# Optimization experiments

Measured on AMD Instinct MI355X. Metric: run time of the kernel, lower is better.

The kernel has to match this reference:

```python
import jax, jax.numpy as jnp
import numpy as np

EPS = 1e-8
HIDDEN = 200


def _dsmall(n, d):
    # torch: d = d*(d>eps) + eps*(d<=eps); n/d
    return n / jnp.where(d > EPS, d, EPS)


def _mp_match(v1, v2, w):
    # v1: (B,S,H); v2: (B,S,H) or (B,H); w: (L,H) -> (B,S,L)
    wt = w.T[None, None]                      # (1,1,H,L)
    a = v1[..., None] * wt                    # (B,S,H,L)
    if v2.ndim == 2:
        v2 = jnp.broadcast_to(v2[:, None, :], v1.shape)
    b = v2[..., None] * wt                    # (B,S,H,L)
    dot = jnp.sum(a * b, axis=2)
    na = jnp.linalg.norm(a, axis=2)
    nb = jnp.linalg.norm(b, axis=2)
    return dot / jnp.maximum(na * nb, EPS)    # cosine_similarity over H


def _mp_pairwise(v1, v2, w):
    # v1: (B,S1,H); v2: (B,S2,H); w: (L,H) -> (B,S1,S2,L)
    a = v1[:, None] * w[None, :, None]        # (B,L,S1,H)
    b = v2[:, None] * w[None, :, None]        # (B,L,S2,H)
    na = jnp.linalg.norm(a, axis=3, keepdims=True)   # (B,L,S1,1)
    nb = jnp.linalg.norm(b, axis=3, keepdims=True)   # (B,L,S2,1)
    n = jnp.einsum('blph,blqh->blpq', a, b)
    d = na * jnp.swapaxes(nb, 2, 3)
    return jnp.transpose(_dsmall(n, d), (0, 2, 3, 1))


def _attention(v1, v2):
    # cosine-similarity matrix (B,S1,S2)
    n1 = jnp.linalg.norm(v1, axis=2, keepdims=True)           # (B,S1,1)
    n2 = jnp.linalg.norm(v2, axis=2, keepdims=True)           # (B,S2,1)
    a = jnp.einsum('bph,bqh->bpq', v1, v2)
    return _dsmall(a, n1 * jnp.swapaxes(n2, 1, 2))


def _matching(con_p, con_h, w1, w2, w3, w4, w5, w6, w7, w8):
    p_fw, p_bw = con_p[..., :HIDDEN], con_p[..., HIDDEN:]
    h_fw, h_bw = con_h[..., :HIDDEN], con_h[..., HIDDEN:]

    # 1) full matching
    mv_p_full_fw = _mp_match(p_fw, h_fw[:, -1, :], w1)
    mv_p_full_bw = _mp_match(p_bw, h_bw[:, 0, :], w2)
    mv_h_full_fw = _mp_match(h_fw, p_fw[:, -1, :], w1)
    mv_h_full_bw = _mp_match(h_bw, p_bw[:, 0, :], w2)

    # 2) maxpooling matching
    mv_max_fw = _mp_pairwise(p_fw, h_fw, w3)  # (B,S1,S2,L)
    mv_max_bw = _mp_pairwise(p_bw, h_bw, w4)
    mv_p_max_fw = jnp.max(mv_max_fw, axis=2)
    mv_p_max_bw = jnp.max(mv_max_bw, axis=2)
    mv_h_max_fw = jnp.max(mv_max_fw, axis=1)
    mv_h_max_bw = jnp.max(mv_max_bw, axis=1)

    # 3) attentive matching (mean)
    att_fw = _attention(p_fw, h_fw)           # (B,S1,S2)
    att_bw = _attention(p_bw, h_bw)

    # sum of att_h over dim 2 is a matmul (same math, no (B,S1,S2,H) tensor)
    att_h_sum_fw = jnp.einsum('bpq,bqh->bph', att_fw, h_fw)
    att_h_sum_bw = jnp.einsum('bpq,bqh->bph', att_bw, h_bw)
    att_p_sum_fw = jnp.einsum('bpq,bph->bqh', att_fw, p_fw)
    att_p_sum_bw = jnp.einsum('bpq,bph->bqh', att_bw, p_bw)

    att_mean_h_fw = _dsmall(att_h_sum_fw, jnp.sum(att_fw, axis=2, keepdims=True))
    att_mean_h_bw = _dsmall(att_h_sum_bw, jnp.sum(att_bw, axis=2, keepdims=True))
    att_mean_p_fw = _dsmall(att_p_sum_fw, jnp.swapaxes(jnp.sum(att_fw, axis=1, keepdims=True), 1, 2))
    att_mean_p_bw = _dsmall(att_p_sum_bw, jnp.swapaxes(jnp.sum(att_bw, axis=1, keepdims=True), 1, 2))

    mv_p_att_mean_fw = _mp_match(p_fw, att_mean_h_fw, w5)
    mv_p_att_mean_bw = _mp_match(p_bw, att_mean_h_bw, w6)
    mv_h_att_mean_fw = _mp_match(h_fw, att_mean_p_fw, w5)
    mv_h_att_mean_bw = _mp_match(h_bw, att_mean_p_bw, w6)

    # 4) max-attentive matching (needs full (B,S1,S2,H) broadcast for the max)
    att_h_fw = h_fw[:, None, :, :] * att_fw[:, :, :, None]   # (B,S1,S2,H)
    att_h_bw = h_bw[:, None, :, :] * att_bw[:, :, :, None]
    att_p_fw = p_fw[:, :, None, :] * att_fw[:, :, :, None]
    att_p_bw = p_bw[:, :, None, :] * att_bw[:, :, :, None]

    att_max_h_fw = jnp.max(att_h_fw, axis=2)                 # (B,S1,H)
    att_max_h_bw = jnp.max(att_h_bw, axis=2)
    att_max_p_fw = jnp.max(att_p_fw, axis=1)                 # (B,S2,H)
    att_max_p_bw = jnp.max(att_p_bw, axis=1)

    mv_p_att_max_fw = _mp_match(p_fw, att_max_h_fw, w7)
    mv_p_att_max_bw = _mp_match(p_bw, att_max_h_bw, w8)
    mv_h_att_max_fw = _mp_match(h_fw, att_max_p_fw, w7)
    mv_h_att_max_bw = _mp_match(h_bw, att_max_p_bw, w8)

    mv_p = jnp.concatenate([mv_p_full_fw, mv_p_max_fw, mv_p_att_mean_fw, mv_p_att_max_fw,
                            mv_p_full_bw, mv_p_max_bw, mv_p_att_mean_bw, mv_p_att_max_bw], axis=2)
    mv_h = jnp.concatenate([mv_h_full_fw, mv_h_max_fw, mv_h_att_mean_fw, mv_h_att_max_fw,
                            mv_h_full_bw, mv_h_max_bw, mv_h_att_mean_bw, mv_h_att_max_bw], axis=2)
    # dropout is identity in inference mode
    return mv_p, mv_h


def setup_inputs() -> dict:
    key = jax.random.key(0)
    ks = jax.random.split(key, 10)
    B, S, H, L = 32, 64, HIDDEN, 20
    w_std = np.sqrt(2.0 / H)  # kaiming_normal fan_in
    inp = {
        'con_p': jax.random.normal(ks[0], (B, S, 2 * H), dtype=jnp.float32),
        'con_h': jax.random.normal(ks[1], (B, S, 2 * H), dtype=jnp.float32),
    }
    for i in range(8):
        inp[f'mp_w{i+1}'] = jax.random.normal(ks[2 + i], (L, H), dtype=jnp.float32) * w_std
    return inp


def reference(con_p, con_h, mp_w1, mp_w2, mp_w3, mp_w4, mp_w5, mp_w6, mp_w7, mp_w8):
    return _matching(con_p, con_h, mp_w1, mp_w2, mp_w3, mp_w4, mp_w5, mp_w6, mp_w7, mp_w8)
```

## Files before the change

kernel.cpp:

```cpp
#include <hip/hip_runtime.h>
#include <hip/hip_bf16.h>
#include <math.h>

#define EPS 1e-8f
#define BB 32
#define SS 64
#define HH 200
#define LL 20
#define KST 232
#define S16ST 72
#define BHST 72
#define MLST 208

typedef short bf16x8 __attribute__((ext_vector_type(8)));
typedef float f32x4 __attribute__((ext_vector_type(4)));
typedef _Float16 f16x8v __attribute__((ext_vector_type(8)));
typedef _Float16 f16x2 __attribute__((ext_vector_type(2)));

__global__ __launch_bounds__(512) void fused_all_kernel(
        const float* __restrict__ conp, const float* __restrict__ conh,
        const float* __restrict__ w1, const float* __restrict__ w2,
        const float* __restrict__ w3, const float* __restrict__ w4,
        const float* __restrict__ w5, const float* __restrict__ w6,
        const float* __restrict__ w7, const float* __restrict__ w8,
        float* __restrict__ out) {
    __shared__ __align__(16) float smem[19104];
    int t = threadIdx.x;

    int wg = ((blockIdx.x & 7) * 224) + (blockIdx.x >> 3);
    int grp = wg / 7;
    int rem = wg % 7;

    if (rem < 2) {
        _Float16* AT16 = (_Float16*)smem;
        _Float16* BT16 = (_Float16*)(smem + 1856);
        _Float16* BHh  = (_Float16*)(smem + 9280);
        _Float16* S16h = (_Float16*)(smem + 16768);
        float* nrmA  = smem + 17344;
        float* nrmB  = smem + 17360;
        _Float16* meanLh = (_Float16*)(smem + 17440);
        _Float16* PB = (_Float16*)smem;
        _Float16* WB = (_Float16*)(smem + 5568);

        int blk = grp * 2 + rem;
        int qh = blk & 3;
        int sdb = blk >> 2;
        int b = sdb & 31, sd = sdb >> 5;
        int dir = sd & 1, side = sd >> 1;
        const float* selfb = side ? conh : conp;
        const float* oppb  = side ? conp : conh;
        int fidx = dir ? 0 : (SS - 1);
        const float* fvr = oppb + (b * SS + fidx) * (2 * HH) + dir * HH;

        int arow = t / 25, ack = t % 25;

        float xr[8], yv0[8];
        if (t < 400) {
            const float* xp = selfb + (b * SS + qh * 16 + arow) * (2 * HH) + dir * HH + ack * 8;
            *(float4*)&xr[0] = *(const float4*)xp; *(float4*)&xr[4] = *(const float4*)(xp + 4);
            *(float4*)&yv0[0] = *(const float4*)(fvr + ack * 8);
            *(float4*)&yv0[4] = *(const float4*)(fvr + ack * 8 + 4);
            f16x8v r8;
#pragma unroll
            for (int i = 0; i < 8; ++i) r8[i] = (_Float16)xr[i];
            *(f16x8v*)&AT16[arow * KST + ack * 8] = r8;
        }
        {
            f16x8v z8 = (f16x8v)(_Float16)0.f;
            if (t < 312) {
                if (t < 48) { int row = t / 3, ckp = 25 + t % 3;
                    *(f16x8v*)&AT16[row * KST + ckp * 8] = z8;
                } else if (t < 240) { int e2 = t - 48; int row = e2 / 3, ckp = 25 + e2 % 3;
                    *(f16x8v*)&BT16[row * KST + ckp * 8] = z8;
                } else { int e2 = t - 240; int row = 200 + e2 / 9, c8 = (e2 % 9) * 8;
                    *(f16x8v*)&BHh[row * BHST + c8] = z8;
                }
            }
        }
        for (int e = t; e < 1600; e += 512) {
            int rw = e / 25, ck = e % 25, k = ck * 8;
            const float* xp = oppb + (b * SS + rw) * (2 * HH) + dir * HH + k;
            float xv[8];
            *(float4*)&xv[0] = *(const float4*)xp; *(float4*)&xv[4] = *(const float4*)(xp + 4);
            f16x8v r8;
#pragma unroll
            for (int i = 0; i < 8; ++i) r8[i] = (_Float16)xv[i];
            *(f16x8v*)&BT16[rw * KST + k] = r8;
        }
        __syncthreads();

        int wv_ = __builtin_amdgcn_readfirstlane(t >> 6);
        int lane = t & 63;
        int q = lane >> 4, c = lane & 15;

        f32x4 accS = (f32x4){0.f, 0.f, 0.f, 0.f};
        if (wv_ < 4) {
            int ct = wv_;
            for (int ks = 0; ks < 7; ++ks) {
                int kb = ks * 32 + q * 8;
                f16x8v af  = *(const f16x8v*)&AT16[c * KST + kb];
                f16x8v bf_ = *(const f16x8v*)&BT16[(ct * 16 + c) * KST + kb];
                accS = __builtin_amdgcn_mfma_f32_16x16x32_f16(af, bf_, accS, 0, 0, 0);
            }
        } else {
            int dt = wv_ - 4;
            f32x4 accB = (f32x4){0.f, 0.f, 0.f, 0.f};
            for (int ks = 0; ks < 7; ++ks) {
                int kb = ks * 32 + q * 8;
                f16x8v bf_ = *(const f16x8v*)&BT16[(dt * 16 + c) * KST + kb];
                accB = __builtin_amdgcn_mfma_f32_16x16x32_f16(bf_, bf_, accB, 0, 0, 0);
            }
            if ((c >> 2) == q) nrmB[dt * 16 + c] = accB[c & 3];
            if (dt == 0) {
                f32x4 accA = (f32x4){0.f, 0.f, 0.f, 0.f};
                for (int ks = 0; ks < 7; ++ks) {
                    int kb = ks * 32 + q * 8;
                    f16x8v af = *(const f16x8v*)&AT16[c * KST + kb];
                    accA = __builtin_amdgcn_mfma_f32_16x16x32_f16(af, af, accA, 0, 0, 0);
                }
                if ((c >> 2) == q) nrmA[c] = accA[c & 3];
            } else {
                for (int ch = dt - 1; ch < 25; ch += 3) {
                    f16x8v v = *(const f16x8v*)&BT16[lane * KST + ch * 8];
#pragma unroll
                    for (int i = 0; i < 8; ++i) BHh[(ch * 8 + i) * BHST + lane] = v[i];
                }
            }
        }
        __syncthreads();

        if (wv_ < 4) {
            int col = wv_ * 16 + c;
            float no = sqrtf(nrmB[col]);
#pragma unroll
            for (int r = 0; r < 4; ++r) {
                int row = q * 4 + r;
                float ns = sqrtf(nrmA[row]);
                S16h[row * S16ST + col] = (_Float16)(accS[r] / fmaxf(ns * no, EPS));
            }
        }
        __syncthreads();

        float wf0[8], wf1[8], wf2[8];
        if (t < 500) {
            int wl = t / 25, wck = t % 25;
            const float* wp0 = (dir ? w2 : w1) + wl * HH + wck * 8;
            const float* wp1 = (dir ? w6 : w5) + wl * HH + wck * 8;
            const float* wp2 = (dir ? w8 : w7) + wl * HH + wck * 8;
            *(float4*)&wf0[0] = *(const float4*)wp0; *(float4*)&wf0[4] = *(const float4*)(wp0 + 4);
            *(float4*)&wf1[0] = *(const float4*)wp1; *(float4*)&wf1[4] = *(const float4*)(wp1 + 4);
            *(float4*)&wf2[0] = *(const float4*)wp2; *(float4*)&wf2[4] = *(const float4*)(wp2 + 4);
        }

        f16x2 mx0, mx1, mx2, mx3;
        {
            f16x2 ninf = {(_Float16)(-INFINITY), (_Float16)(-INFINITY)};
            mx0 = ninf; mx1 = ninf; mx2 = ninf; mx3 = ninf;
        }
        if (wv_ == 7) {
            for (int nt = 0; nt < 13; ++nt) {
                f32x4 macc = (f32x4){0.f, 0.f, 0.f, 0.f};
#pragma unroll
                for (int k2 = 0; k2 < 2; ++k2) {
                    int kb = k2 * 32 + q * 8;
                    f16x8v sa = *(const f16x8v*)&S16h[c * S16ST + kb];
                    f16x8v bh = *(const f16x8v*)&BHh[(nt * 16 + c) * BHST + kb];
                    macc = __builtin_amdgcn_mfma_f32_16x16x32_f16(sa, bh, macc, 0, 0, 0);
                }
                int h = nt * 16 + c;
                if (h < 200) {
#pragma unroll
                    for (int r = 0; r < 4; ++r)
                        meanLh[(q * 4 + r) * MLST + h] = (_Float16)(macc[r] * 0.125f);
                }
            }
        } else if (t < 400) {
            const _Float16* srow = &S16h[arow * S16ST];
            const _Float16* bcol = &BT16[ack * 8];
            for (int kg = 0; kg < 8; ++kg) {
                f16x8v sr = *(const f16x8v*)&srow[kg * 8];
#pragma unroll
                for (int kk = 0; kk < 8; ++kk) {
                    _Float16 sh = sr[kk];
                    f16x2 sv = {sh, sh};
                    f16x8v bv = *(const f16x8v*)&bcol[(kg * 8 + kk) * KST];
                    f16x2 p0 = sv * __builtin_shufflevector(bv, bv, 0, 1);
                    f16x2 p1 = sv * __builtin_shufflevector(bv, bv, 2, 3);
                    f16x2 p2 = sv * __builtin_shufflevector(bv, bv, 4, 5);
                    f16x2 p3 = sv * __builtin_shufflevector(bv, bv, 6, 7);
                    mx0 = __builtin_elementwise_max(mx0, p0);
                    mx1 = __builtin_elementwise_max(mx1, p1);
                    mx2 = __builtin_elementwise_max(mx2, p2);
                    mx3 = __builtin_elementwise_max(mx3, p3);
                }
            }
        }
        __syncthreads();

#pragma unroll
        for (int m = 0; m < 3; ++m) {
            if (t < 400) {
                float yv[8];
                if (m == 0) {
#pragma unroll
                    for (int i = 0; i < 8; ++i) yv[i] = yv0[i];
                } else if (m == 1) {
                    f16x8v yl = *(const f16x8v*)&meanLh[arow * MLST + ack * 8];
#pragma unroll
                    for (int i = 0; i < 8; ++i) yv[i] = (float)yl[i];
                } else {
                    yv[0] = (float)mx0[0]; yv[1] = (float)mx0[1];
                    yv[2] = (float)mx1[0]; yv[3] = (float)mx1[1];
                    yv[4] = (float)mx2[0]; yv[5] = (float)mx2[1];
                    yv[6] = (float)mx3[0]; yv[7] = (float)mx3[1];
                }
                f16x8v r1, r2;
#pragma unroll
                for (int i = 0; i < 8; ++i) {
                    r1[i] = (_Float16)(xr[i] * yv[i]);
                    r2[i] = (_Float16)(yv[i] * yv[i]);
                }
                if (m == 0) {
                    f16x8v r0;
#pragma unroll
                    for (int i = 0; i < 8; ++i) r0[i] = (_Float16)(xr[i] * xr[i]);
                    *(f16x8v*)&PB[(0 * 16 + arow) * KST + ack * 8] = r0;
                }
                *(f16x8v*)&PB[(1 * 16 + arow) * KST + ack * 8] = r1;
                *(f16x8v*)&PB[(2 * 16 + arow) * KST + ack * 8] = r2;
            }
            if (t < 500) {
                int wl = t / 25, wck = t % 25;
                f16x8v wr;
                if (m == 0) {
#pragma unroll
                    for (int i = 0; i < 8; ++i) wr[i] = (_Float16)(wf0[i] * wf0[i]);
                } else if (m == 1) {
#pragma unroll
                    for (int i = 0; i < 8; ++i) wr[i] = (_Float16)(wf1[i] * wf1[i]);
                } else {
#pragma unroll
                    for (int i = 0; i < 8; ++i) wr[i] = (_Float16)(wf2[i] * wf2[i]);
                }
                *(f16x8v*)&WB[wl * KST + wck * 8] = wr;
            }
            if (m == 0) {
                f16x8v z8 = (f16x8v)(_Float16)0.f;
                for (int e = t; e < 540; e += 512) {
                    if (e < 144) { int row = e / 3, ckp = 25 + e % 3;
                        *(f16x8v*)&PB[row * KST + ckp * 8] = z8;
                    } else if (e < 480) { int e2 = e - 144; int row = 20 + e2 / 28, ckp = e2 % 28;
                        *(f16x8v*)&WB[row * KST + ckp * 8] = z8;
                    } else { int e2 = e - 480; int row = e2 / 3, ckp = 25 + e2 % 3;
                        *(f16x8v*)&WB[row * KST + ckp * 8] = z8;
                    }
                }
            }
            __syncthreads();

            if (wv_ < 2) {
                int ntile = wv_;
                f32x4 accA = (f32x4){0.f, 0.f, 0.f, 0.f};
                f32x4 accD = (f32x4){0.f, 0.f, 0.f, 0.f};
                f32x4 accB = (f32x4){0.f, 0.f, 0.f, 0.f};
                for (int ks = 0; ks < 7; ++ks) {
                    int kb = ks * 32 + q * 8;
                    f16x8v bfw = *(const f16x8v*)&WB[(ntile * 16 + c) * KST + kb];
                    f16x8v a0 = *(const f16x8v*)&PB[(0 * 16 + c) * KST + kb];
                    f16x8v a1 = *(const f16x8v*)&PB[(1 * 16 + c) * KST + kb];
                    f16x8v a2 = *(const f16x8v*)&PB[(2 * 16 + c) * KST + kb];
                    accA = __builtin_amdgcn_mfma_f32_16x16x32_f16(a0, bfw, accA, 0, 0, 0);
                    accD = __builtin_amdgcn_mfma_f32_16x16x32_f16(a1, bfw, accD, 0, 0, 0);
                    accB = __builtin_amdgcn_mfma_f32_16x16x32_f16(a2, bfw, accB, 0, 0, 0);
                }
                int l_ = ntile * 16 + c;
                if (l_ < LL) {
                    int chunk = (m == 0) ? 0 : (m == 1) ? 40 : 60;
#pragma unroll
                    for (int r = 0; r < 4; ++r) {
                        int s = qh * 16 + q * 4 + r;
                        float cosv = accD[r] / fmaxf(sqrtf(accA[r] * accB[r]), EPS);
                        out[side * (BB * SS * 160) + (b * SS + s) * 160 + dir * 80 + chunk + l_] = cosv;
                    }
                }
            }
            if (m < 2) __syncthreads();
        }
    } else {
        __hip_bfloat16* AT = (__hip_bfloat16*)smem;
        __hip_bfloat16* BT = (__hip_bfloat16*)(smem + 7424);
        float* cmL = smem + 14848;
        float* nA  = smem + 15104;
        float* nB  = smem + 15168;
        int blk = grp * 5 + (rem - 2);
        int l = blk % LL; int db = blk / LL; int b = db & 31; int dir = db >> 5;

        const float* wrow = (dir ? w4 : w3) + l * HH;
        const float* Ag = conp + dir * HH;
        const float* Bg = conh + dir * HH;

        for (int e = t; e < 64 * 28; e += 512) {
            int m = e / 28, ck = e - m * 28;
            int k = ck * 8;
            __align__(16) __hip_bfloat16 at8[8];
            __align__(16) __hip_bfloat16 bt8[8];
            if (k < HH) {
                const float* ap = Ag + (b * SS + m) * (2 * HH) + k;
                const float* bp = Bg + (b * SS + m) * (2 * HH) + k;
                const float* wp = wrow + k;
                float av[8], bv[8], wvv[8];
                *(float4*)&av[0]  = *(const float4*)ap; *(float4*)&av[4]  = *(const float4*)(ap + 4);
                *(float4*)&bv[0]  = *(const float4*)bp; *(float4*)&bv[4]  = *(const float4*)(bp + 4);
                *(float4*)&wvv[0] = *(const float4*)wp; *(float4*)&wvv[4] = *(const float4*)(wp + 4);
#pragma unroll
                for (int i = 0; i < 8; ++i) {
                    at8[i] = __float2bfloat16(av[i] * wvv[i]);
                    bt8[i] = __float2bfloat16(bv[i] * wvv[i]);
                }
            } else {
#pragma unroll
                for (int ii = 0; ii < 8; ++ii) { at8[ii] = __float2bfloat16(0.f); bt8[ii] = __float2bfloat16(0.f); }
            }
            *(bf16x8*)&AT[m * KST + k] = *(bf16x8*)at8;
            *(bf16x8*)&BT[m * KST + k] = *(bf16x8*)bt8;
        }
        __syncthreads();

        int wv_ = __builtin_amdgcn_readfirstlane(t >> 6);
        int lane = t & 63;
        int q = lane >> 4, c = lane & 15;
        int m0 = wv_ * 16;

        f32x4 acc[4];
#pragma unroll
        for (int ct = 0; ct < 4; ++ct) acc[ct] = (f32x4){0.f, 0.f, 0.f, 0.f};

        if (wv_ < 4) {
            for (int ks = 0; ks < 7; ++ks) {
                int kb = ks * 32 + q * 8;
                bf16x8 af = *(const bf16x8*)&AT[(m0 + c) * KST + kb];
#pragma unroll
                for (int ct = 0; ct < 4; ++ct) {
                    bf16x8 bf_ = *(const bf16x8*)&BT[(ct * 16 + c) * KST + kb];
                    acc[ct] = __builtin_amdgcn_mfma_f32_16x16x32_bf16(af, bf_, acc[ct], 0, 0, 0);
                }
            }
        } else {
            int d0 = (wv_ - 4) * 16;
            f32x4 accA = (f32x4){0.f, 0.f, 0.f, 0.f};
            f32x4 accB = (f32x4){0.f, 0.f, 0.f, 0.f};
            for (int ks = 0; ks < 7; ++ks) {
                int kb = ks * 32 + q * 8;
                bf16x8 af = *(const bf16x8*)&AT[(d0 + c) * KST + kb];
                bf16x8 bf_ = *(const bf16x8*)&BT[(d0 + c) * KST + kb];
                accA = __builtin_amdgcn_mfma_f32_16x16x32_bf16(af, af, accA, 0, 0, 0);
                accB = __builtin_amdgcn_mfma_f32_16x16x32_bf16(bf_, bf_, accB, 0, 0, 0);
            }
            if ((c >> 2) == q) { nA[d0 + c] = accA[c & 3]; nB[d0 + c] = accB[c & 3]; }
        }
        __syncthreads();

        if (wv_ < 4) {
            float na[4], nb[4];
#pragma unroll
            for (int r = 0; r < 4; ++r) na[r] = sqrtf(nA[m0 + q * 4 + r]);
#pragma unroll
            for (int ct = 0; ct < 4; ++ct) nb[ct] = sqrtf(nB[ct * 16 + c]);

            float rowm[4] = {-INFINITY, -INFINITY, -INFINITY, -INFINITY};
            float colm[4] = {-INFINITY, -INFINITY, -INFINITY, -INFINITY};
#pragma unroll
            for (int ct = 0; ct < 4; ++ct) {
#pragma unroll
                for (int r = 0; r < 4; ++r) {
                    float cv = acc[ct][r] / fmaxf(na[r] * nb[ct], EPS);
                    rowm[r] = fmaxf(rowm[r], cv);
                    colm[ct] = fmaxf(colm[ct], cv);
                }
            }

#pragma unroll
            for (int r = 0; r < 4; ++r) {
                float v = rowm[r];
                v = fmaxf(v, __shfl_xor(v, 1, 64));
                v = fmaxf(v, __shfl_xor(v, 2, 64));
                v = fmaxf(v, __shfl_xor(v, 4, 64));
                v = fmaxf(v, __shfl_xor(v, 8, 64));
                rowm[r] = v;
            }
            if (c == 0) {
#pragma unroll
                for (int r = 0; r < 4; ++r) {
                    int i = m0 + q * 4 + r;
                    out[(b * SS + i) * 160 + dir * 80 + 20 + l] = rowm[r];
                }
            }

#pragma unroll
            for (int ct = 0; ct < 4; ++ct) {
                float v = colm[ct];
                v = fmaxf(v, __shfl_xor(v, 16, 64));
                v = fmaxf(v, __shfl_xor(v, 32, 64));
                colm[ct] = v;
            }
            if (q == 0) {
#pragma unroll
                for (int ct = 0; ct < 4; ++ct) cmL[wv_ * 64 + ct * 16 + c] = colm[ct];
            }
        }
        __syncthreads();
        if (t < 64) {
            float m = fmaxf(fmaxf(cmL[t], cmL[64 + t]), fmaxf(cmL[128 + t], cmL[192 + t]));
            out[BB * SS * 160 + (b * SS + t) * 160 + dir * 80 + 20 + l] = m;
        }
    }
}

extern "C" void kernel_launch(void* const* d_in, const int* in_sizes, int n_in,
                              void* d_out, int out_size, void* d_ws, size_t ws_size,
                              hipStream_t stream) {
    const float* conp = (const float*)d_in[0];
    const float* conh = (const float*)d_in[1];
    const float* w1 = (const float*)d_in[2];
    const float* w2 = (const float*)d_in[3];
    const float* w3 = (const float*)d_in[4];
    const float* w4 = (const float*)d_in[5];
    const float* w5 = (const float*)d_in[6];
    const float* w6 = (const float*)d_in[7];
    const float* w7 = (const float*)d_in[8];
    const float* w8 = (const float*)d_in[9];
    float* out = (float*)d_out;
    (void)d_ws; (void)ws_size;

    fused_all_kernel<<<1792, 512, 0, stream>>>(conp, conh,
                                               w1, w2, w3, w4, w5, w6, w7, w8, out);
}
```

Measured before the change: 107.4 us.

## Batch five perspectives per maxpool block with fp16 raw inputs and w² scaling

The maxpool-matching branch now handles five perspective rows per workgroup instead of one. It stages the raw p/h rows once as fp16 plus the squared weights, and forms a*w² in registers before each MFMA. This cuts redundant global loads and conversions of the same inputs across perspectives, and the grid shrinks from 1792 to 768 blocks with a minimum-occupancy launch bound. The trade-offs are more MFMA work per block, fewer blocks for load balance, and different precision (fp16 with w² instead of bf16 with w applied to both sides).

```diff
diff --git a/kernel.cpp b/kernel.cpp
--- a/kernel.cpp
+++ b/kernel.cpp
@@ -17,7 +17,7 @@
 typedef _Float16 f16x8v __attribute__((ext_vector_type(8)));
 typedef _Float16 f16x2 __attribute__((ext_vector_type(2)));
 
-__global__ __launch_bounds__(512) void fused_all_kernel(
+__global__ __launch_bounds__(512, 4) void fused_all_kernel(
         const float* __restrict__ conp, const float* __restrict__ conh,
         const float* __restrict__ w1, const float* __restrict__ w2,
         const float* __restrict__ w3, const float* __restrict__ w4,
@@ -27,9 +27,9 @@
     __shared__ __align__(16) float smem[19104];
     int t = threadIdx.x;
 
-    int wg = ((blockIdx.x & 7) * 224) + (blockIdx.x >> 3);
-    int grp = wg / 7;
-    int rem = wg % 7;
+    int wg = ((blockIdx.x & 7) * 96) + (blockIdx.x >> 3);
+    int grp = wg / 3;
+    int rem = wg % 3;
 
     if (rem < 2) {
         _Float16* AT16 = (_Float16*)smem;
@@ -287,132 +287,182 @@
             if (m < 2) __syncthreads();
         }
     } else {
-        __hip_bfloat16* AT = (__hip_bfloat16*)smem;
-        __hip_bfloat16* BT = (__hip_bfloat16*)(smem + 7424);
-        float* cmL = smem + 14848;
-        float* nA  = smem + 15104;
-        float* nB  = smem + 15168;
-        int blk = grp * 5 + (rem - 2);
-        int l = blk % LL; int db = blk / LL; int b = db & 31; int dir = db >> 5;
-
-        const float* wrow = (dir ? w4 : w3) + l * HH;
+        _Float16* ATr = (_Float16*)smem;
+        _Float16* BTr = (_Float16*)(smem + 7424);
+        _Float16* w2L = (_Float16*)(smem + 14848);
+        float* nA5  = smem + 15432;
+        float* nB5  = smem + 15752;
+        float* cmL5 = smem + 16072;
+
+        int cblk = grp;
+        int lg = cblk & 3;
+        int db = cblk >> 2;
+        int b = db & 31, dir = db >> 5;
+        int l0 = lg * 5;
+        const float* wsrc = dir ? w4 : w3;
         const float* Ag = conp + dir * HH;
         const float* Bg = conh + dir * HH;
 
-        for (int e = t; e < 64 * 28; e += 512) {
-            int m = e / 28, ck = e - m * 28;
-            int k = ck * 8;
-            __align__(16) __hip_bfloat16 at8[8];
-            __align__(16) __hip_bfloat16 bt8[8];
-            if (k < HH) {
-                const float* ap = Ag + (b * SS + m) * (2 * HH) + k;
-                const float* bp = Bg + (b * SS + m) * (2 * HH) + k;
-                const float* wp = wrow + k;
-                float av[8], bv[8], wvv[8];
-                *(float4*)&av[0]  = *(const float4*)ap; *(float4*)&av[4]  = *(const float4*)(ap + 4);
-                *(float4*)&bv[0]  = *(const float4*)bp; *(float4*)&bv[4]  = *(const float4*)(bp + 4);
+        for (int e = t; e < 3200; e += 512) {
+            int half = (e >= 1600) ? 1 : 0;
+            int e2 = e - half * 1600;
+            int rw = e2 / 25, ck = e2 % 25, k = ck * 8;
+            const float* xp = (half ? Bg : Ag) + (b * SS + rw) * (2 * HH) + k;
+            float xv[8];
+            *(float4*)&xv[0] = *(const float4*)xp; *(float4*)&xv[4] = *(const float4*)(xp + 4);
+            f16x8v r8;
+#pragma unroll
+            for (int i = 0; i < 8; ++i) r8[i] = (_Float16)xv[i];
+            _Float16* dst = half ? BTr : ATr;
+            *(f16x8v*)&dst[rw * KST + k] = r8;
+        }
+        {
+            f16x8v z8 = (f16x8v)(_Float16)0.f;
+            if (t < 384) {
+                int half = (t >= 192) ? 1 : 0;
+                int e2 = t - half * 192;
+                int row = e2 / 3, ckp = 25 + e2 % 3;
+                _Float16* dst = half ? BTr : ATr;
+                *(f16x8v*)&dst[row * KST + ckp * 8] = z8;
+            } else if (t < 399) {
+                int e2 = t - 384;
+                int wl = e2 / 3, ckp = 25 + e2 % 3;
+                *(f16x8v*)&w2L[wl * KST + ckp * 8] = z8;
+            }
+            if (t < 125) {
+                int wl = t / 25, wck = t % 25;
+                const float* wp = wsrc + (l0 + wl) * HH + wck * 8;
+                float wvv[8];
                 *(float4*)&wvv[0] = *(const float4*)wp; *(float4*)&wvv[4] = *(const float4*)(wp + 4);
-#pragma unroll
-                for (int i = 0; i < 8; ++i) {
-                    at8[i] = __float2bfloat16(av[i] * wvv[i]);
-                    bt8[i] = __float2bfloat16(bv[i] * wvv[i]);
-                }
-            } else {
-#pragma unroll
-                for (int ii = 0; ii < 8; ++ii) { at8[ii] = __float2bfloat16(0.f); bt8[ii] = __float2bfloat16(0.f); }
-            }
-            *(bf16x8*)&AT[m * KST + k] = *(bf16x8*)at8;
-            *(bf16x8*)&BT[m * KST + k] = *(bf16x8*)bt8;
+                f16x8v r8;
+#pragma unroll
+                for (int i = 0; i < 8; ++i) r8[i] = (_Float16)(wvv[i] * wvv[i]);
+                *(f16x8v*)&w2L[wl * KST + wck * 8] = r8;
+            }
         }
         __syncthreads();
 
         int wv_ = __builtin_amdgcn_readfirstlane(t >> 6);
         int lane = t & 63;
         int q = lane >> 4, c = lane & 15;
-        int m0 = wv_ * 16;
-
-        f32x4 acc[4];
-#pragma unroll
-        for (int ct = 0; ct < 4; ++ct) acc[ct] = (f32x4){0.f, 0.f, 0.f, 0.f};
+        int m0 = (wv_ & 3) * 16;
+
+        f32x4 z4 = (f32x4){0.f, 0.f, 0.f, 0.f};
+        f32x4 acc0[4] = {z4, z4, z4, z4};
+        f32x4 acc1[4] = {z4, z4, z4, z4};
+        f32x4 acc2[4] = {z4, z4, z4, z4};
 
         if (wv_ < 4) {
             for (int ks = 0; ks < 7; ++ks) {
                 int kb = ks * 32 + q * 8;
-                bf16x8 af = *(const bf16x8*)&AT[(m0 + c) * KST + kb];
+                f16x8v ar  = *(const f16x8v*)&ATr[(m0 + c) * KST + kb];
+                f16x8v ww0 = *(const f16x8v*)&w2L[0 * KST + kb];
+                f16x8v ww1 = *(const f16x8v*)&w2L[1 * KST + kb];
+                f16x8v ww2 = *(const f16x8v*)&w2L[2 * KST + kb];
+                f16x8v af0 = ar * ww0, af1 = ar * ww1, af2 = ar * ww2;
 #pragma unroll
                 for (int ct = 0; ct < 4; ++ct) {
-                    bf16x8 bf_ = *(const bf16x8*)&BT[(ct * 16 + c) * KST + kb];
-                    acc[ct] = __builtin_amdgcn_mfma_f32_16x16x32_bf16(af, bf_, acc[ct], 0, 0, 0);
+                    f16x8v br = *(const f16x8v*)&BTr[(ct * 16 + c) * KST + kb];
+                    acc0[ct] = __builtin_amdgcn_mfma_f32_16x16x32_f16(af0, br, acc0[ct], 0, 0, 0);
+                    acc1[ct] = __builtin_amdgcn_mfma_f32_16x16x32_f16(af1, br, acc1[ct], 0, 0, 0);
+                    acc2[ct] = __builtin_amdgcn_mfma_f32_16x16x32_f16(af2, br, acc2[ct], 0, 0, 0);
                 }
             }
         } else {
             int d0 = (wv_ - 4) * 16;
-            f32x4 accA = (f32x4){0.f, 0.f, 0.f, 0.f};
-            f32x4 accB = (f32x4){0.f, 0.f, 0.f, 0.f};
+            f32x4 nacA[5] = {z4, z4, z4, z4, z4};
+            f32x4 nacB[5] = {z4, z4, z4, z4, z4};
             for (int ks = 0; ks < 7; ++ks) {
                 int kb = ks * 32 + q * 8;
-                bf16x8 af = *(const bf16x8*)&AT[(d0 + c) * KST + kb];
-                bf16x8 bf_ = *(const bf16x8*)&BT[(d0 + c) * KST + kb];
-                accA = __builtin_amdgcn_mfma_f32_16x16x32_bf16(af, af, accA, 0, 0, 0);
-                accB = __builtin_amdgcn_mfma_f32_16x16x32_bf16(bf_, bf_, accB, 0, 0, 0);
-            }
-            if ((c >> 2) == q) { nA[d0 + c] = accA[c & 3]; nB[d0 + c] = accB[c & 3]; }
-        }
-        __syncthreads();
+                f16x8v ar = *(const f16x8v*)&ATr[(d0 + c) * KST + kb];
+                f16x8v br = *(const f16x8v*)&BTr[(d0 + c) * KST + kb];
+#pragma unroll
+                for (int li = 0; li < 5; ++li) {
+                    f16x8v wf = *(const f16x8v*)&w2L[li * KST + kb];
+                    f16x8v afw = ar * wf;
+                    f16x8v bfw = br * wf;
+                    nacA[li] = __builtin_amdgcn_mfma_f32_16x16x32_f16(afw, ar, nacA[li], 0, 0, 0);
+                    nacB[li] = __builtin_amdgcn_mfma_f32_16x16x32_f16(bfw, br, nacB[li], 0, 0, 0);
+                }
+            }
+            if ((c >> 2) == q) {
+#pragma unroll
+                for (int li = 0; li < 5; ++li) {
+                    nA5[li * 64 + d0 + c] = nacA[li][c & 3];
+                    nB5[li * 64 + d0 + c] = nacB[li][c & 3];
+                }
+            }
+        }
+        __syncthreads();
+
+#define C_EPI(LI, ACC) do { \
+    float na_[4], nb_[4]; \
+    _Pragma("unroll") for (int r_ = 0; r_ < 4; ++r_) na_[r_] = sqrtf(nA5[(LI) * 64 + m0 + q * 4 + r_]); \
+    _Pragma("unroll") for (int ct_ = 0; ct_ < 4; ++ct_) nb_[ct_] = sqrtf(nB5[(LI) * 64 + ct_ * 16 + c]); \
+    float rowm_[4] = {-INFINITY, -INFINITY, -INFINITY, -INFINITY}; \
+    float colm_[4] = {-INFINITY, -INFINITY, -INFINITY, -INFINITY}; \
+    _Pragma("unroll") for (int ct_ = 0; ct_ < 4; ++ct_) { \
+        _Pragma("unroll") for (int r_ = 0; r_ < 4; ++r_) { \
+            float cv_ = (ACC)[ct_][r_] / fmaxf(na_[r_] * nb_[ct_], EPS); \
+            rowm_[r_] = fmaxf(rowm_[r_], cv_); \
+            colm_[ct_] = fmaxf(colm_[ct_], cv_); \
+        } \
+    } \
+    _Pragma("unroll") for (int r_ = 0; r_ < 4; ++r_) { \
+        float v_ = rowm_[r_]; \
+        v_ = fmaxf(v_, __shfl_xor(v_, 1, 64)); \
+        v_ = fmaxf(v_, __shfl_xor(v_, 2, 64)); \
+        v_ = fmaxf(v_, __shfl_xor(v_, 4, 64)); \
+        v_ = fmaxf(v_, __shfl_xor(v_, 8, 64)); \
+        rowm_[r_] = v_; \
+    } \
+    if (c == 0) { \
+        _Pragma("unroll") for (int r_ = 0; r_ < 4; ++r_) \
+            out[(b * SS + m0 + q * 4 + r_) * 160 + dir * 80 + 20 + l0 + (LI)] = rowm_[r_]; \
+    } \
+    _Pragma("unroll") for (int ct_ = 0; ct_ < 4; ++ct_) { \
+        float v_ = colm_[ct_]; \
+        v_ = fmaxf(v_, __shfl_xor(v_, 16, 64)); \
+        v_ = fmaxf(v_, __shfl_xor(v_, 32, 64)); \
+        colm_[ct_] = v_; \
+    } \
+    if (q == 0) { \
+        _Pragma("unroll") for (int ct_ = 0; ct_ < 4; ++ct_) \
+            cmL5[(LI) * 256 + wv_ * 64 + ct_ * 16 + c] = colm_[ct_]; \
+    } \
+} while (0)
 
         if (wv_ < 4) {
-            float na[4], nb[4];
-#pragma unroll
-            for (int r = 0; r < 4; ++r) na[r] = sqrtf(nA[m0 + q * 4 + r]);
-#pragma unroll
-            for (int ct = 0; ct < 4; ++ct) nb[ct] = sqrtf(nB[ct * 16 + c]);
-
-            float rowm[4] = {-INFINITY, -INFINITY, -INFINITY, -INFINITY};
-            float colm[4] = {-INFINITY, -INFINITY, -INFINITY, -INFINITY};
-#pragma unroll
-            for (int ct = 0; ct < 4; ++ct) {
-#pragma unroll
-                for (int r = 0; r < 4; ++r) {
-                    float cv = acc[ct][r] / fmaxf(na[r] * nb[ct], EPS);
-                    rowm[r] = fmaxf(rowm[r], cv);
-                    colm[ct] = fmaxf(colm[ct], cv);
-                }
-            }
-
-#pragma unroll
-            for (int r = 0; r < 4; ++r) {
-                float v = rowm[r];
-                v = fmaxf(v, __shfl_xor(v, 1, 64));
-                v = fmaxf(v, __shfl_xor(v, 2, 64));
-                v = fmaxf(v, __shfl_xor(v, 4, 64));
-                v = fmaxf(v, __shfl_xor(v, 8, 64));
-                rowm[r] = v;
-            }
-            if (c == 0) {
-#pragma unroll
-                for (int r = 0; r < 4; ++r) {
-                    int i = m0 + q * 4 + r;
-                    out[(b * SS + i) * 160 + dir * 80 + 20 + l] = rowm[r];
-                }
-            }
-
-#pragma unroll
-            for (int ct = 0; ct < 4; ++ct) {
-                float v = colm[ct];
-                v = fmaxf(v, __shfl_xor(v, 16, 64));
-                v = fmaxf(v, __shfl_xor(v, 32, 64));
-                colm[ct] = v;
-            }
-            if (q == 0) {
-#pragma unroll
-                for (int ct = 0; ct < 4; ++ct) cmL[wv_ * 64 + ct * 16 + c] = colm[ct];
-            }
-        }
-        __syncthreads();
-        if (t < 64) {
-            float m = fmaxf(fmaxf(cmL[t], cmL[64 + t]), fmaxf(cmL[128 + t], cmL[192 + t]));
-            out[BB * SS * 160 + (b * SS + t) * 160 + dir * 80 + 20 + l] = m;
-        }
+            C_EPI(0, acc0);
+            C_EPI(1, acc1);
+            C_EPI(2, acc2);
+            f32x4 acc3[4] = {z4, z4, z4, z4};
+            f32x4 acc4[4] = {z4, z4, z4, z4};
+            for (int ks = 0; ks < 7; ++ks) {
+                int kb = ks * 32 + q * 8;
+                f16x8v ar  = *(const f16x8v*)&ATr[(m0 + c) * KST + kb];
+                f16x8v ww3 = *(const f16x8v*)&w2L[3 * KST + kb];
+                f16x8v ww4 = *(const f16x8v*)&w2L[4 * KST + kb];
+                f16x8v af3 = ar * ww3, af4 = ar * ww4;
+#pragma unroll
+                for (int ct = 0; ct < 4; ++ct) {
+                    f16x8v br = *(const f16x8v*)&BTr[(ct * 16 + c) * KST + kb];
+                    acc3[ct] = __builtin_amdgcn_mfma_f32_16x16x32_f16(af3, br, acc3[ct], 0, 0, 0);
+                    acc4[ct] = __builtin_amdgcn_mfma_f32_16x16x32_f16(af4, br, acc4[ct], 0, 0, 0);
+                }
+            }
+            C_EPI(3, acc3);
+            C_EPI(4, acc4);
+        }
+        __syncthreads();
+
+        if (t < 320) {
+            int li = t >> 6, j = t & 63;
+            const float* cm = &cmL5[li * 256];
+            float mm = fmaxf(fmaxf(cm[j], cm[64 + j]), fmaxf(cm[128 + j], cm[192 + j]));
+            out[BB * SS * 160 + (b * SS + j) * 160 + dir * 80 + 20 + l0 + li] = mm;
+        }
+#undef C_EPI
     }
 }
 
@@ -432,6 +482,6 @@
     float* out = (float*)d_out;
     (void)d_ws; (void)ws_size;
 
-    fused_all_kernel<<<1792, 512, 0, stream>>>(conp, conh,
-                                               w1, w2, w3, w4, w5, w6, w7, w8, out);
+    fused_all_kernel<<<768, 512, 0, stream>>>(conp, conh,
+                                              w1, w2, w3, w4, w5, w6, w7, w8, out);
 }
```

Measured after the change: 101.7 us. 5.3% less time.
